# Optimization experiments

Measured on AMD Instinct MI355X. Metric: run time of the kernel, lower is better.

Reference implementation:

```python
import jax, jax.numpy as jnp
import numpy as np

N_NODES = 100000
N_EDGES = 1600000
F_IN = 128
HEADS = 4
C_OUT = 32
NEG_SLOPE = 0.2


def setup_inputs() -> dict:
    key = jax.random.key(0)
    k1, k2, k3, k4, k5, k6 = jax.random.split(key, 6)
    x = jax.random.normal(k1, (N_NODES, F_IN), dtype=jnp.float32)
    edge_index = jax.random.randint(k2, (2, N_EDGES), 0, N_NODES, dtype=jnp.int64)
    # glorot-ish scales
    W = jax.random.normal(k3, (F_IN, HEADS * C_OUT), dtype=jnp.float32) * (1.0 / np.sqrt(F_IN))
    att_src = jax.random.normal(k4, (HEADS, C_OUT), dtype=jnp.float32) * (1.0 / np.sqrt(C_OUT))
    att_dst = jax.random.normal(k5, (HEADS, C_OUT), dtype=jnp.float32) * (1.0 / np.sqrt(C_OUT))
    bias = jnp.zeros((HEADS * C_OUT,), dtype=jnp.float32)
    return {"x": x, "edge_index": edge_index, "W": W,
            "att_src": att_src, "att_dst": att_dst, "bias": bias}


def _gat_forward(x, edge_index, W, att_src, att_dst, bias):
    N = x.shape[0]
    H, C = att_src.shape
    h = (x @ W).reshape(N, H, C)                      # [N,H,C]
    # PyG GATConv default: add self-loops
    loops = jnp.arange(N, dtype=edge_index.dtype)
    src = jnp.concatenate([edge_index[0], loops])     # [E+N]
    dst = jnp.concatenate([edge_index[1], loops])
    a_src = jnp.einsum("nhc,hc->nh", h, att_src)      # [N,H]
    a_dst = jnp.einsum("nhc,hc->nh", h, att_dst)
    e = jax.nn.leaky_relu(a_src[src] + a_dst[dst], NEG_SLOPE)  # [E+N,H]
    # segment softmax over destination node (every node has a self-loop)
    m = jax.ops.segment_max(e, dst, num_segments=N)
    e = jnp.exp(e - m[dst])
    s = jax.ops.segment_sum(e, dst, num_segments=N)
    alpha = e / (s[dst] + 1e-16)                      # [E+N,H]
    msg = h[src] * alpha[:, :, None]                  # [E+N,H,C]
    out = jax.ops.segment_sum(msg, dst, num_segments=N).reshape(N, H * C)
    return jnp.tanh(out + bias)


def reference(x, edge_index, W, att_src, att_dst, bias):
    return _gat_forward(x, edge_index, W, att_src, att_dst, bias)
```

## Files before the change

kernel.cpp:

```cpp
#include <hip/hip_runtime.h>
#include <math.h>

#define NN 100000
#define NE 1600000
#define F_IN 128
#define HEADS 4
#define HC 128
#define NEG_SLOPE 0.2f
#define NBKT 391
#define BCAP 5120
#define LDK 136

typedef __attribute__((ext_vector_type(8))) short bf16x8;
typedef __attribute__((ext_vector_type(4))) float f32x4;

static __device__ __forceinline__ short f2bf_rne(float f) {
    unsigned u = __float_as_uint(f);
    unsigned r = (u + 0x7FFFu + ((u >> 16) & 1u)) >> 16;
    return (short)r;
}
static __device__ __forceinline__ float bf2f(short s) {
    return __uint_as_float(((unsigned)(unsigned short)s) << 16);
}

__global__ __launch_bounds__(256) void prep_kernel(
        const float* __restrict__ W, short* __restrict__ wt_hi, short* __restrict__ wt_lo,
        const int* __restrict__ ei, int* __restrict__ flag, int* __restrict__ bcur) {
    if (blockIdx.x == 0 && threadIdx.x < 64) {
        int l = threadIdx.x;
        int v = ei[2 * l + 1];
        for (int off = 1; off < 64; off <<= 1) v |= __shfl_xor(v, off);
        if (l == 0) *flag = (v == 0) ? 1 : 0;
    }
    if (blockIdx.x == 1 || blockIdx.x == 2) {
        int z = (blockIdx.x - 1) * 256 + threadIdx.x;
        if (z < NBKT) bcur[z] = 0;
    }
    int i = blockIdx.x * 256 + threadIdx.x;
    if (i >= F_IN * HC) return;
    int k = i >> 7, n = i & 127;
    float f = W[k * HC + n];
    short hb = f2bf_rne(f);
    wt_hi[n * F_IN + k] = hb;
    wt_lo[n * F_IN + k] = f2bf_rne(f - bf2f(hb));
}

__global__ __launch_bounds__(256) void mfma_gemm_kernel(
        const float* __restrict__ x, const short* __restrict__ wt_hi,
        const short* __restrict__ wt_lo, const float* __restrict__ att_src,
        const float* __restrict__ att_dst, unsigned short* __restrict__ h_bf,
        float* __restrict__ a_src, float* __restrict__ a_dst) {
    __shared__ short lw_hi[64 * LDK];
    __shared__ short lw_lo[64 * LDK];
    int t = threadIdx.x;
    int nh = blockIdx.x & 1;
    int blk = blockIdx.x >> 1;

    for (int c = t; c < 1024; c += 256) {
        int n = c >> 4;
        int kk = (c & 15) * 8;
        bf16x8 vh = *(const bf16x8*)(wt_hi + (nh * 64 + n) * F_IN + kk);
        bf16x8 vl = *(const bf16x8*)(wt_lo + (nh * 64 + n) * F_IN + kk);
        *(bf16x8*)(lw_hi + n * LDK + kk) = vh;
        *(bf16x8*)(lw_lo + n * LDK + kk) = vl;
    }
    __syncthreads();

    int strip = blk * 4 + (t >> 6);
    if (strip >= NN / 16) return;
    int lane = t & 63;
    int l15 = lane & 15;
    int q = lane >> 4;

    f32x4 acc[4];
#pragma unroll
    for (int nt = 0; nt < 4; ++nt) acc[nt] = (f32x4){0.f, 0.f, 0.f, 0.f};

    const float* xp = x + (size_t)(strip * 16 + l15) * F_IN + q * 8;

#pragma unroll
    for (int ki = 0; ki < 4; ++ki) {
        float4 v0 = *(const float4*)(xp + ki * 32);
        float4 v1 = *(const float4*)(xp + ki * 32 + 4);
        float vv[8] = {v0.x, v0.y, v0.z, v0.w, v1.x, v1.y, v1.z, v1.w};
        bf16x8 a_hi, a_lo;
#pragma unroll
        for (int j = 0; j < 8; ++j) {
            short hb = f2bf_rne(vv[j]);
            a_hi[j] = hb;
            a_lo[j] = f2bf_rne(vv[j] - bf2f(hb));
        }
        int koff = ki * 32 + q * 8;
#pragma unroll
        for (int nt = 0; nt < 4; ++nt) {
            int lidx = (nt * 16 + l15) * LDK + koff;
            bf16x8 b_hi = *(const bf16x8*)(lw_hi + lidx);
            bf16x8 b_lo = *(const bf16x8*)(lw_lo + lidx);
            acc[nt] = __builtin_amdgcn_mfma_f32_16x16x32_bf16(a_hi, b_hi, acc[nt], 0, 0, 0);
            acc[nt] = __builtin_amdgcn_mfma_f32_16x16x32_bf16(a_lo, b_hi, acc[nt], 0, 0, 0);
            acc[nt] = __builtin_amdgcn_mfma_f32_16x16x32_bf16(a_hi, b_lo, acc[nt], 0, 0, 0);
        }
    }

    int orow = strip * 16 + q * 4;
    int cbase = nh * 64;
#pragma unroll
    for (int nt = 0; nt < 4; ++nt)
#pragma unroll
        for (int r = 0; r < 4; ++r)
            h_bf[(size_t)(orow + r) * HC + cbase + nt * 16 + l15] =
                (unsigned short)f2bf_rne(acc[nt][r]);

#pragma unroll
    for (int hl = 0; hl < 2; ++hl) {
        int hd = nh * 2 + hl;
        float as0 = att_src[hd * 32 + l15];
        float as1 = att_src[hd * 32 + 16 + l15];
        float ad0 = att_dst[hd * 32 + l15];
        float ad1 = att_dst[hd * 32 + 16 + l15];
#pragma unroll
        for (int r = 0; r < 4; ++r) {
            float ps = acc[2 * hl][r] * as0 + acc[2 * hl + 1][r] * as1;
            float pd = acc[2 * hl][r] * ad0 + acc[2 * hl + 1][r] * ad1;
#pragma unroll
            for (int off = 1; off < 16; off <<= 1) {
                ps += __shfl_xor(ps, off);
                pd += __shfl_xor(pd, off);
            }
            if (l15 == 0) {
                int row = orow + r;
                a_src[row * 4 + hd] = ps;
                a_dst[row * 4 + hd] = pd;
            }
        }
    }
}

__global__ __launch_bounds__(256) void bucket_scatter_kernel(
        const int* __restrict__ ei, const int* __restrict__ flag,
        int* __restrict__ bcur, unsigned* __restrict__ pairs) {
    __shared__ int lhist[NBKT];
    __shared__ int gbase[NBKT];
    int t = threadIdx.x;
    for (int i = t; i < NBKT; i += 256) lhist[i] = 0;
    __syncthreads();
    int is64 = *flag;
    int base = blockIdx.x * 4096;

    unsigned wrd[16];
    int meta[16];
#pragma unroll
    for (int it = 0; it < 16; ++it) {
        int e = base + it * 256 + t;
        if (e < NE) {
            int src = is64 ? ei[2 * e] : ei[e];
            int dst = is64 ? ei[2 * NE + 2 * e] : ei[NE + e];
            int b = dst >> 8;
            int r = atomicAdd(&lhist[b], 1);
            wrd[it] = (unsigned)src | ((unsigned)(dst & 255) << 17);
            meta[it] = b | (r << 9);
        } else {
            meta[it] = -1;
        }
    }
    __syncthreads();
    for (int i = t; i < NBKT; i += 256)
        gbase[i] = lhist[i] ? atomicAdd(&bcur[i], lhist[i]) : 0;
    __syncthreads();
#pragma unroll
    for (int it = 0; it < 16; ++it) {
        if (meta[it] >= 0) {
            int b = meta[it] & 511;
            int r = meta[it] >> 9;
            pairs[(size_t)b * BCAP + gbase[b] + r] = wrd[it];
        }
    }
}

__global__ __launch_bounds__(256) void bucket_csr_kernel(
        const int* __restrict__ bcur, const unsigned* __restrict__ pairs,
        const float* __restrict__ a_src, const float* __restrict__ a_dst,
        int* __restrict__ deg, int* __restrict__ offsets,
        int* __restrict__ csr_src, unsigned* __restrict__ wal,
        float2* __restrict__ selfdata) {
    __shared__ unsigned lpairs[BCAP];
    __shared__ int sd[256];
    __shared__ int cnt256[256];
    __shared__ int lcur[256];
    __shared__ float sumw[1024];

    int b = blockIdx.x;
    int t = threadIdx.x;
    int node = (b << 8) + t;

    int partial = 0;
    for (int i = t; i < b; i += 256) partial += bcur[i];
    sd[t] = partial;
    __syncthreads();
    for (int off = 128; off > 0; off >>= 1) {
        if (t < off) sd[t] += sd[t + off];
        __syncthreads();
    }
    int bktbase = sd[0];
    __syncthreads();

    cnt256[t] = 0;
    for (int i = t; i < 1024; i += 256) sumw[i] = 0.f;
    __syncthreads();

    int cnt = bcur[b];
    const unsigned* __restrict__ bp = pairs + (size_t)b * BCAP;
    for (int i = t; i < cnt; i += 256) {
        unsigned w = bp[i];
        lpairs[i] = w;
        atomicAdd(&cnt256[w >> 17], 1);
    }
    __syncthreads();

    int v = cnt256[t];
    sd[t] = v;
    __syncthreads();
    for (int off = 1; off < 256; off <<= 1) {
        int u = (t >= off) ? sd[t - off] : 0;
        __syncthreads();
        sd[t] += u;
        __syncthreads();
    }
    int myoff = bktbase + sd[t] - v;
    if (node < NN) {
        deg[node] = v;
        offsets[node] = myoff;
    }
    lcur[t] = myoff;
    __syncthreads();

    for (int i = t; i < cnt; i += 256) {
        unsigned w = lpairs[i];
        int src = (int)(w & 0x1FFFFu);
        int dl = (int)(w >> 17);
        float4 as = ((const float4*)a_src)[src];
        float4 ad = ((const float4*)a_dst)[(b << 8) + dl];
        float e0 = as.x + ad.x; e0 = (e0 < 0.f) ? NEG_SLOPE * e0 : e0;
        float e1 = as.y + ad.y; e1 = (e1 < 0.f) ? NEG_SLOPE * e1 : e1;
        float e2 = as.z + ad.z; e2 = (e2 < 0.f) ? NEG_SLOPE * e2 : e2;
        float e3 = as.w + ad.w; e3 = (e3 < 0.f) ? NEG_SLOPE * e3 : e3;
        float w0 = __expf(e0), w1 = __expf(e1), w2 = __expf(e2), w3 = __expf(e3);
        int pos = atomicAdd(&lcur[dl], 1);
        csr_src[pos] = src;
        unsigned lo = (unsigned)(unsigned short)f2bf_rne(w0) |
                      ((unsigned)(unsigned short)f2bf_rne(w1) << 16);
        unsigned hi = (unsigned)(unsigned short)f2bf_rne(w2) |
                      ((unsigned)(unsigned short)f2bf_rne(w3) << 16);
        ((uint2*)wal)[pos] = make_uint2(lo, hi);
        atomicAdd(&sumw[dl * 4 + 0], w0);
        atomicAdd(&sumw[dl * 4 + 1], w1);
        atomicAdd(&sumw[dl * 4 + 2], w2);
        atomicAdd(&sumw[dl * 4 + 3], w3);
    }
    __syncthreads();

    if (node < NN) {
        float4 as = ((const float4*)a_src)[node];
        float4 ad = ((const float4*)a_dst)[node];
        float sf[4];
        float e0 = as.x + ad.x; e0 = (e0 < 0.f) ? NEG_SLOPE * e0 : e0; sf[0] = __expf(e0);
        float e1 = as.y + ad.y; e1 = (e1 < 0.f) ? NEG_SLOPE * e1 : e1; sf[1] = __expf(e1);
        float e2 = as.z + ad.z; e2 = (e2 < 0.f) ? NEG_SLOPE * e2 : e2; sf[2] = __expf(e2);
        float e3 = as.w + ad.w; e3 = (e3 < 0.f) ? NEG_SLOPE * e3 : e3; sf[3] = __expf(e3);
#pragma unroll
        for (int hd = 0; hd < 4; ++hd) {
            float tot = sumw[t * 4 + hd] + sf[hd];
            float inv = 1.f / (tot + 1e-16f);
            selfdata[node * 4 + hd] = make_float2(inv, sf[hd] * inv);
        }
    }
}

__global__ __launch_bounds__(256) void gat_aggr_kernel(
        const int* __restrict__ offsets, const int* __restrict__ deg,
        const int* __restrict__ csr_src, const unsigned* __restrict__ wal,
        const float2* __restrict__ selfdata,
        const unsigned* __restrict__ h2, const float* __restrict__ bias,
        float* __restrict__ out) {
    int wid = (blockIdx.x * 256 + threadIdx.x) >> 6;
    int dst = __builtin_amdgcn_readfirstlane(wid);
    if (dst >= NN) return;
    int lane = threadIdx.x & 63;
    int hd = lane >> 4;
    unsigned hsel2 = (unsigned)(hd & 2);
    unsigned hsel1 = (unsigned)(hd & 1);

    int start = offsets[dst];
    int n = deg[dst];
    float2 sdta = selfdata[dst * 4 + hd];

    float accx = 0.f, accy = 0.f;
    int j = 0;
    for (; j + 3 < n; j += 4) {
        int base = start + j;
        int s0 = csr_src[base + 0];
        int s1 = csr_src[base + 1];
        int s2 = csr_src[base + 2];
        int s3 = csr_src[base + 3];
        uint2 wv0 = ((const uint2*)wal)[base + 0];
        uint2 wv1 = ((const uint2*)wal)[base + 1];
        uint2 wv2 = ((const uint2*)wal)[base + 2];
        uint2 wv3 = ((const uint2*)wal)[base + 3];
        unsigned u0 = h2[(size_t)s0 * 64 + lane];
        unsigned u1 = h2[(size_t)s1 * 64 + lane];
        unsigned u2 = h2[(size_t)s2 * 64 + lane];
        unsigned u3 = h2[(size_t)s3 * 64 + lane];
        unsigned ws0 = hsel2 ? wv0.y : wv0.x;
        unsigned ws1 = hsel2 ? wv1.y : wv1.x;
        unsigned ws2 = hsel2 ? wv2.y : wv2.x;
        unsigned ws3 = hsel2 ? wv3.y : wv3.x;
        float w0 = __uint_as_float(hsel1 ? (ws0 & 0xFFFF0000u) : (ws0 << 16));
        float w1 = __uint_as_float(hsel1 ? (ws1 & 0xFFFF0000u) : (ws1 << 16));
        float w2 = __uint_as_float(hsel1 ? (ws2 & 0xFFFF0000u) : (ws2 << 16));
        float w3 = __uint_as_float(hsel1 ? (ws3 & 0xFFFF0000u) : (ws3 << 16));
        accx += w0 * __uint_as_float(u0 << 16);
        accy += w0 * __uint_as_float(u0 & 0xFFFF0000u);
        accx += w1 * __uint_as_float(u1 << 16);
        accy += w1 * __uint_as_float(u1 & 0xFFFF0000u);
        accx += w2 * __uint_as_float(u2 << 16);
        accy += w2 * __uint_as_float(u2 & 0xFFFF0000u);
        accx += w3 * __uint_as_float(u3 << 16);
        accy += w3 * __uint_as_float(u3 & 0xFFFF0000u);
    }
    for (; j < n; ++j) {
        int base = start + j;
        int s0 = csr_src[base];
        uint2 wv0 = ((const uint2*)wal)[base];
        unsigned u0 = h2[(size_t)s0 * 64 + lane];
        unsigned ws0 = hsel2 ? wv0.y : wv0.x;
        float w0 = __uint_as_float(hsel1 ? (ws0 & 0xFFFF0000u) : (ws0 << 16));
        accx += w0 * __uint_as_float(u0 << 16);
        accy += w0 * __uint_as_float(u0 & 0xFFFF0000u);
    }

    unsigned us = h2[(size_t)dst * 64 + lane];
    float2 b2 = ((const float2*)bias)[lane];
    float ox = tanhf(accx * sdta.x + sdta.y * __uint_as_float(us << 16) + b2.x);
    float oy = tanhf(accy * sdta.x + sdta.y * __uint_as_float(us & 0xFFFF0000u) + b2.y);
    ((float2*)out)[(size_t)dst * 64 + lane] = make_float2(ox, oy);
}

extern "C" void kernel_launch(void* const* d_in, const int* in_sizes, int n_in,
                              void* d_out, int out_size, void* d_ws, size_t ws_size,
                              hipStream_t stream) {
    const float* x       = (const float*)d_in[0];
    const int*   ei      = (const int*)  d_in[1];
    const float* W       = (const float*)d_in[2];
    const float* att_src = (const float*)d_in[3];
    const float* att_dst = (const float*)d_in[4];
    const float* bias    = (const float*)d_in[5];
    float* out = (float*)d_out;

    unsigned short* h_bf = (unsigned short*)d_ws;
    float* a_src = (float*)(h_bf + (size_t)NN * HC);
    float* a_dst = a_src + (size_t)NN * HEADS;
    short* wt_hi = (short*)(a_dst + (size_t)NN * HEADS);
    short* wt_lo = wt_hi + F_IN * HC;
    int* flag    = (int*)(wt_lo + F_IN * HC);
    int* bcur    = flag + 4;
    int* deg     = bcur + NBKT + 1;
    int* offsets = deg + NN;
    int* csr_src = offsets + NN;
    unsigned* wal = (unsigned*)(csr_src + NE);
    float2* selfdata = (float2*)(wal + (size_t)NE * 2);
    unsigned* pairs = (unsigned*)(selfdata + (size_t)NN * HEADS);

    hipLaunchKernelGGL(prep_kernel, dim3(64), dim3(256), 0, stream,
                       W, wt_hi, wt_lo, ei, flag, bcur);

    hipLaunchKernelGGL(bucket_scatter_kernel, dim3((NE + 4095) / 4096), dim3(256), 0, stream,
                       ei, flag, bcur, pairs);

    hipLaunchKernelGGL(mfma_gemm_kernel, dim3(1563 * 2), dim3(256), 0, stream,
                       x, wt_hi, wt_lo, att_src, att_dst, h_bf, a_src, a_dst);

    hipLaunchKernelGGL(bucket_csr_kernel, dim3(NBKT), dim3(256), 0, stream,
                       bcur, pairs, a_src, a_dst, deg, offsets, csr_src, wal, selfdata);

    hipLaunchKernelGGL(gat_aggr_kernel, dim3(NN * 64 / 256), dim3(256), 0, stream,
                       offsets, deg, csr_src, wal, selfdata,
                       (const unsigned*)h_bf, bias, out);
}
```

Measured before the change: 279.3 us.

## Compute full GEMM rows per block, move softmax denominators into aggregation kernel

The GEMM kernel now computes all 128 output columns per strip, so x is read and split into bf16 hi/lo only once; it reloads the second half of W into the same LDS between the two halves and raises launch bounds to hint higher occupancy. The CSR-building kernel no longer accumulates per-node softmax sums with LDS atomics and no longer writes selfdata. Instead the aggregation kernel sums the edge weights itself and computes the self-loop term from a_src/a_dst. The aggregation loop also gains an 8-way unrolled path for more outstanding gathers. The trade-off is extra registers (8 accumulators plus cached A fragments) and a second LDS fill with syncs in the GEMM. The denominator is now summed from bf16-rounded weights, which changes rounding slightly.

```diff
diff --git a/kernel.cpp b/kernel.cpp
--- a/kernel.cpp
+++ b/kernel.cpp
@@ -10,6 +10,7 @@
 #define NBKT 391
 #define BCAP 5120
 #define LDK 136
+#define NSTRIP 6250
 
 typedef __attribute__((ext_vector_type(8))) short bf16x8;
 typedef __attribute__((ext_vector_type(4))) float f32x4;
@@ -45,7 +46,7 @@
     wt_lo[n * F_IN + k] = f2bf_rne(f - bf2f(hb));
 }
 
-__global__ __launch_bounds__(256) void mfma_gemm_kernel(
+__global__ __launch_bounds__(256, 4) void mfma_gemm_kernel(
         const float* __restrict__ x, const short* __restrict__ wt_hi,
         const short* __restrict__ wt_lo, const float* __restrict__ att_src,
         const float* __restrict__ att_dst, unsigned short* __restrict__ h_bf,
@@ -53,42 +54,40 @@
     __shared__ short lw_hi[64 * LDK];
     __shared__ short lw_lo[64 * LDK];
     int t = threadIdx.x;
-    int nh = blockIdx.x & 1;
-    int blk = blockIdx.x >> 1;
+    int blk = blockIdx.x;
 
     for (int c = t; c < 1024; c += 256) {
         int n = c >> 4;
         int kk = (c & 15) * 8;
-        bf16x8 vh = *(const bf16x8*)(wt_hi + (nh * 64 + n) * F_IN + kk);
-        bf16x8 vl = *(const bf16x8*)(wt_lo + (nh * 64 + n) * F_IN + kk);
-        *(bf16x8*)(lw_hi + n * LDK + kk) = vh;
-        *(bf16x8*)(lw_lo + n * LDK + kk) = vl;
+        *(bf16x8*)(lw_hi + n * LDK + kk) = *(const bf16x8*)(wt_hi + n * F_IN + kk);
+        *(bf16x8*)(lw_lo + n * LDK + kk) = *(const bf16x8*)(wt_lo + n * F_IN + kk);
     }
     __syncthreads();
 
     int strip = blk * 4 + (t >> 6);
-    if (strip >= NN / 16) return;
+    int valid = strip < NSTRIP;
+    int sclamp = valid ? strip : NSTRIP - 1;
     int lane = t & 63;
     int l15 = lane & 15;
     int q = lane >> 4;
 
-    f32x4 acc[4];
-#pragma unroll
-    for (int nt = 0; nt < 4; ++nt) acc[nt] = (f32x4){0.f, 0.f, 0.f, 0.f};
-
-    const float* xp = x + (size_t)(strip * 16 + l15) * F_IN + q * 8;
+    f32x4 acc[8];
+#pragma unroll
+    for (int nt = 0; nt < 8; ++nt) acc[nt] = (f32x4){0.f, 0.f, 0.f, 0.f};
+
+    bf16x8 ah[4], al[4];
+    const float* xp = x + (size_t)(sclamp * 16 + l15) * F_IN + q * 8;
 
 #pragma unroll
     for (int ki = 0; ki < 4; ++ki) {
         float4 v0 = *(const float4*)(xp + ki * 32);
         float4 v1 = *(const float4*)(xp + ki * 32 + 4);
         float vv[8] = {v0.x, v0.y, v0.z, v0.w, v1.x, v1.y, v1.z, v1.w};
-        bf16x8 a_hi, a_lo;
 #pragma unroll
         for (int j = 0; j < 8; ++j) {
             short hb = f2bf_rne(vv[j]);
-            a_hi[j] = hb;
-            a_lo[j] = f2bf_rne(vv[j] - bf2f(hb));
+            ah[ki][j] = hb;
+            al[ki][j] = f2bf_rne(vv[j] - bf2f(hb));
         }
         int koff = ki * 32 + q * 8;
 #pragma unroll
@@ -96,32 +95,55 @@
             int lidx = (nt * 16 + l15) * LDK + koff;
             bf16x8 b_hi = *(const bf16x8*)(lw_hi + lidx);
             bf16x8 b_lo = *(const bf16x8*)(lw_lo + lidx);
-            acc[nt] = __builtin_amdgcn_mfma_f32_16x16x32_bf16(a_hi, b_hi, acc[nt], 0, 0, 0);
-            acc[nt] = __builtin_amdgcn_mfma_f32_16x16x32_bf16(a_lo, b_hi, acc[nt], 0, 0, 0);
-            acc[nt] = __builtin_amdgcn_mfma_f32_16x16x32_bf16(a_hi, b_lo, acc[nt], 0, 0, 0);
-        }
-    }
+            acc[nt] = __builtin_amdgcn_mfma_f32_16x16x32_bf16(ah[ki], b_hi, acc[nt], 0, 0, 0);
+            acc[nt] = __builtin_amdgcn_mfma_f32_16x16x32_bf16(al[ki], b_hi, acc[nt], 0, 0, 0);
+            acc[nt] = __builtin_amdgcn_mfma_f32_16x16x32_bf16(ah[ki], b_lo, acc[nt], 0, 0, 0);
+        }
+    }
+
+    __syncthreads();
+    for (int c = t; c < 1024; c += 256) {
+        int n = c >> 4;
+        int kk = (c & 15) * 8;
+        *(bf16x8*)(lw_hi + n * LDK + kk) = *(const bf16x8*)(wt_hi + (64 + n) * F_IN + kk);
+        *(bf16x8*)(lw_lo + n * LDK + kk) = *(const bf16x8*)(wt_lo + (64 + n) * F_IN + kk);
+    }
+    __syncthreads();
+
+#pragma unroll
+    for (int ki = 0; ki < 4; ++ki) {
+        int koff = ki * 32 + q * 8;
+#pragma unroll
+        for (int nt = 0; nt < 4; ++nt) {
+            int lidx = (nt * 16 + l15) * LDK + koff;
+            bf16x8 b_hi = *(const bf16x8*)(lw_hi + lidx);
+            bf16x8 b_lo = *(const bf16x8*)(lw_lo + lidx);
+            acc[4 + nt] = __builtin_amdgcn_mfma_f32_16x16x32_bf16(ah[ki], b_hi, acc[4 + nt], 0, 0, 0);
+            acc[4 + nt] = __builtin_amdgcn_mfma_f32_16x16x32_bf16(al[ki], b_hi, acc[4 + nt], 0, 0, 0);
+            acc[4 + nt] = __builtin_amdgcn_mfma_f32_16x16x32_bf16(ah[ki], b_lo, acc[4 + nt], 0, 0, 0);
+        }
+    }
+
+    if (!valid) return;
 
     int orow = strip * 16 + q * 4;
-    int cbase = nh * 64;
-#pragma unroll
-    for (int nt = 0; nt < 4; ++nt)
+#pragma unroll
+    for (int nt = 0; nt < 8; ++nt)
 #pragma unroll
         for (int r = 0; r < 4; ++r)
-            h_bf[(size_t)(orow + r) * HC + cbase + nt * 16 + l15] =
+            h_bf[(size_t)(orow + r) * HC + nt * 16 + l15] =
                 (unsigned short)f2bf_rne(acc[nt][r]);
 
 #pragma unroll
-    for (int hl = 0; hl < 2; ++hl) {
-        int hd = nh * 2 + hl;
+    for (int hd = 0; hd < 4; ++hd) {
         float as0 = att_src[hd * 32 + l15];
         float as1 = att_src[hd * 32 + 16 + l15];
         float ad0 = att_dst[hd * 32 + l15];
         float ad1 = att_dst[hd * 32 + 16 + l15];
 #pragma unroll
         for (int r = 0; r < 4; ++r) {
-            float ps = acc[2 * hl][r] * as0 + acc[2 * hl + 1][r] * as1;
-            float pd = acc[2 * hl][r] * ad0 + acc[2 * hl + 1][r] * ad1;
+            float ps = acc[2 * hd][r] * as0 + acc[2 * hd + 1][r] * as1;
+            float pd = acc[2 * hd][r] * ad0 + acc[2 * hd + 1][r] * ad1;
 #pragma unroll
             for (int off = 1; off < 16; off <<= 1) {
                 ps += __shfl_xor(ps, off);
@@ -181,13 +203,11 @@
         const int* __restrict__ bcur, const unsigned* __restrict__ pairs,
         const float* __restrict__ a_src, const float* __restrict__ a_dst,
         int* __restrict__ deg, int* __restrict__ offsets,
-        int* __restrict__ csr_src, unsigned* __restrict__ wal,
-        float2* __restrict__ selfdata) {
+        int* __restrict__ csr_src, unsigned* __restrict__ wal) {
     __shared__ unsigned lpairs[BCAP];
     __shared__ int sd[256];
     __shared__ int cnt256[256];
     __shared__ int lcur[256];
-    __shared__ float sumw[1024];
 
     int b = blockIdx.x;
     int t = threadIdx.x;
@@ -205,7 +225,6 @@
     __syncthreads();
 
     cnt256[t] = 0;
-    for (int i = t; i < 1024; i += 256) sumw[i] = 0.f;
     __syncthreads();
 
     int cnt = bcur[b];
@@ -252,34 +271,13 @@
         unsigned hi = (unsigned)(unsigned short)f2bf_rne(w2) |
                       ((unsigned)(unsigned short)f2bf_rne(w3) << 16);
         ((uint2*)wal)[pos] = make_uint2(lo, hi);
-        atomicAdd(&sumw[dl * 4 + 0], w0);
-        atomicAdd(&sumw[dl * 4 + 1], w1);
-        atomicAdd(&sumw[dl * 4 + 2], w2);
-        atomicAdd(&sumw[dl * 4 + 3], w3);
-    }
-    __syncthreads();
-
-    if (node < NN) {
-        float4 as = ((const float4*)a_src)[node];
-        float4 ad = ((const float4*)a_dst)[node];
-        float sf[4];
-        float e0 = as.x + ad.x; e0 = (e0 < 0.f) ? NEG_SLOPE * e0 : e0; sf[0] = __expf(e0);
-        float e1 = as.y + ad.y; e1 = (e1 < 0.f) ? NEG_SLOPE * e1 : e1; sf[1] = __expf(e1);
-        float e2 = as.z + ad.z; e2 = (e2 < 0.f) ? NEG_SLOPE * e2 : e2; sf[2] = __expf(e2);
-        float e3 = as.w + ad.w; e3 = (e3 < 0.f) ? NEG_SLOPE * e3 : e3; sf[3] = __expf(e3);
-#pragma unroll
-        for (int hd = 0; hd < 4; ++hd) {
-            float tot = sumw[t * 4 + hd] + sf[hd];
-            float inv = 1.f / (tot + 1e-16f);
-            selfdata[node * 4 + hd] = make_float2(inv, sf[hd] * inv);
-        }
     }
 }
 
 __global__ __launch_bounds__(256) void gat_aggr_kernel(
         const int* __restrict__ offsets, const int* __restrict__ deg,
         const int* __restrict__ csr_src, const unsigned* __restrict__ wal,
-        const float2* __restrict__ selfdata,
+        const float* __restrict__ a_src, const float* __restrict__ a_dst,
         const unsigned* __restrict__ h2, const float* __restrict__ bias,
         float* __restrict__ out) {
     int wid = (blockIdx.x * 256 + threadIdx.x) >> 6;
@@ -292,10 +290,69 @@
 
     int start = offsets[dst];
     int n = deg[dst];
-    float2 sdta = selfdata[dst * 4 + hd];
-
-    float accx = 0.f, accy = 0.f;
+
+    float accx = 0.f, accy = 0.f, wsum = 0.f;
     int j = 0;
+    for (; j + 7 < n; j += 8) {
+        int base = start + j;
+        int s0 = csr_src[base + 0];
+        int s1 = csr_src[base + 1];
+        int s2 = csr_src[base + 2];
+        int s3 = csr_src[base + 3];
+        int s4 = csr_src[base + 4];
+        int s5 = csr_src[base + 5];
+        int s6 = csr_src[base + 6];
+        int s7 = csr_src[base + 7];
+        uint2 wv0 = ((const uint2*)wal)[base + 0];
+        uint2 wv1 = ((const uint2*)wal)[base + 1];
+        uint2 wv2 = ((const uint2*)wal)[base + 2];
+        uint2 wv3 = ((const uint2*)wal)[base + 3];
+        uint2 wv4 = ((const uint2*)wal)[base + 4];
+        uint2 wv5 = ((const uint2*)wal)[base + 5];
+        uint2 wv6 = ((const uint2*)wal)[base + 6];
+        uint2 wv7 = ((const uint2*)wal)[base + 7];
+        unsigned u0 = h2[(size_t)s0 * 64 + lane];
+        unsigned u1 = h2[(size_t)s1 * 64 + lane];
+        unsigned u2 = h2[(size_t)s2 * 64 + lane];
+        unsigned u3 = h2[(size_t)s3 * 64 + lane];
+        unsigned u4 = h2[(size_t)s4 * 64 + lane];
+        unsigned u5 = h2[(size_t)s5 * 64 + lane];
+        unsigned u6 = h2[(size_t)s6 * 64 + lane];
+        unsigned u7 = h2[(size_t)s7 * 64 + lane];
+        unsigned ws0 = hsel2 ? wv0.y : wv0.x;
+        unsigned ws1 = hsel2 ? wv1.y : wv1.x;
+        unsigned ws2 = hsel2 ? wv2.y : wv2.x;
+        unsigned ws3 = hsel2 ? wv3.y : wv3.x;
+        unsigned ws4 = hsel2 ? wv4.y : wv4.x;
+        unsigned ws5 = hsel2 ? wv5.y : wv5.x;
+        unsigned ws6 = hsel2 ? wv6.y : wv6.x;
+        unsigned ws7 = hsel2 ? wv7.y : wv7.x;
+        float w0 = __uint_as_float(hsel1 ? (ws0 & 0xFFFF0000u) : (ws0 << 16));
+        float w1 = __uint_as_float(hsel1 ? (ws1 & 0xFFFF0000u) : (ws1 << 16));
+        float w2 = __uint_as_float(hsel1 ? (ws2 & 0xFFFF0000u) : (ws2 << 16));
+        float w3 = __uint_as_float(hsel1 ? (ws3 & 0xFFFF0000u) : (ws3 << 16));
+        float w4 = __uint_as_float(hsel1 ? (ws4 & 0xFFFF0000u) : (ws4 << 16));
+        float w5 = __uint_as_float(hsel1 ? (ws5 & 0xFFFF0000u) : (ws5 << 16));
+        float w6 = __uint_as_float(hsel1 ? (ws6 & 0xFFFF0000u) : (ws6 << 16));
+        float w7 = __uint_as_float(hsel1 ? (ws7 & 0xFFFF0000u) : (ws7 << 16));
+        wsum += ((w0 + w1) + (w2 + w3)) + ((w4 + w5) + (w6 + w7));
+        accx += w0 * __uint_as_float(u0 << 16);
+        accy += w0 * __uint_as_float(u0 & 0xFFFF0000u);
+        accx += w1 * __uint_as_float(u1 << 16);
+        accy += w1 * __uint_as_float(u1 & 0xFFFF0000u);
+        accx += w2 * __uint_as_float(u2 << 16);
+        accy += w2 * __uint_as_float(u2 & 0xFFFF0000u);
+        accx += w3 * __uint_as_float(u3 << 16);
+        accy += w3 * __uint_as_float(u3 & 0xFFFF0000u);
+        accx += w4 * __uint_as_float(u4 << 16);
+        accy += w4 * __uint_as_float(u4 & 0xFFFF0000u);
+        accx += w5 * __uint_as_float(u5 << 16);
+        accy += w5 * __uint_as_float(u5 & 0xFFFF0000u);
+        accx += w6 * __uint_as_float(u6 << 16);
+        accy += w6 * __uint_as_float(u6 & 0xFFFF0000u);
+        accx += w7 * __uint_as_float(u7 << 16);
+        accy += w7 * __uint_as_float(u7 & 0xFFFF0000u);
+    }
     for (; j + 3 < n; j += 4) {
         int base = start + j;
         int s0 = csr_src[base + 0];
@@ -318,6 +375,7 @@
         float w1 = __uint_as_float(hsel1 ? (ws1 & 0xFFFF0000u) : (ws1 << 16));
         float w2 = __uint_as_float(hsel1 ? (ws2 & 0xFFFF0000u) : (ws2 << 16));
         float w3 = __uint_as_float(hsel1 ? (ws3 & 0xFFFF0000u) : (ws3 << 16));
+        wsum += (w0 + w1) + (w2 + w3);
         accx += w0 * __uint_as_float(u0 << 16);
         accy += w0 * __uint_as_float(u0 & 0xFFFF0000u);
         accx += w1 * __uint_as_float(u1 << 16);
@@ -334,14 +392,20 @@
         unsigned u0 = h2[(size_t)s0 * 64 + lane];
         unsigned ws0 = hsel2 ? wv0.y : wv0.x;
         float w0 = __uint_as_float(hsel1 ? (ws0 & 0xFFFF0000u) : (ws0 << 16));
+        wsum += w0;
         accx += w0 * __uint_as_float(u0 << 16);
         accy += w0 * __uint_as_float(u0 & 0xFFFF0000u);
     }
 
+    float e = a_src[dst * 4 + hd] + a_dst[dst * 4 + hd];
+    e = (e < 0.f) ? NEG_SLOPE * e : e;
+    float sf = __expf(e);
+    float inv = 1.f / (wsum + sf + 1e-16f);
+
     unsigned us = h2[(size_t)dst * 64 + lane];
     float2 b2 = ((const float2*)bias)[lane];
-    float ox = tanhf(accx * sdta.x + sdta.y * __uint_as_float(us << 16) + b2.x);
-    float oy = tanhf(accy * sdta.x + sdta.y * __uint_as_float(us & 0xFFFF0000u) + b2.y);
+    float ox = tanhf((accx + sf * __uint_as_float(us << 16)) * inv + b2.x);
+    float oy = tanhf((accy + sf * __uint_as_float(us & 0xFFFF0000u)) * inv + b2.y);
     ((float2*)out)[(size_t)dst * 64 + lane] = make_float2(ox, oy);
 }
 
@@ -367,8 +431,7 @@
     int* offsets = deg + NN;
     int* csr_src = offsets + NN;
     unsigned* wal = (unsigned*)(csr_src + NE);
-    float2* selfdata = (float2*)(wal + (size_t)NE * 2);
-    unsigned* pairs = (unsigned*)(selfdata + (size_t)NN * HEADS);
+    unsigned* pairs = (unsigned*)(wal + (size_t)NE * 2);
 
     hipLaunchKernelGGL(prep_kernel, dim3(64), dim3(256), 0, stream,
                        W, wt_hi, wt_lo, ei, flag, bcur);
@@ -376,13 +439,13 @@
     hipLaunchKernelGGL(bucket_scatter_kernel, dim3((NE + 4095) / 4096), dim3(256), 0, stream,
                        ei, flag, bcur, pairs);
 
-    hipLaunchKernelGGL(mfma_gemm_kernel, dim3(1563 * 2), dim3(256), 0, stream,
+    hipLaunchKernelGGL(mfma_gemm_kernel, dim3(1563), dim3(256), 0, stream,
                        x, wt_hi, wt_lo, att_src, att_dst, h_bf, a_src, a_dst);
 
     hipLaunchKernelGGL(bucket_csr_kernel, dim3(NBKT), dim3(256), 0, stream,
-                       bcur, pairs, a_src, a_dst, deg, offsets, csr_src, wal, selfdata);
+                       bcur, pairs, a_src, a_dst, deg, offsets, csr_src, wal);
 
     hipLaunchKernelGGL(gat_aggr_kernel, dim3(NN * 64 / 256), dim3(256), 0, stream,
-                       offsets, deg, csr_src, wal, selfdata,
+                       offsets, deg, csr_src, wal, a_src, a_dst,
                        (const unsigned*)h_bf, bias, out);
 }
```

Measured after the change: 258.9 us. 1.08x faster.
